# Kernel optimization log

Measured on AMD Instinct MI355X. Metric: run time of the kernel, lower is better.

Reference implementation:

```python
import jax, jax.numpy as jnp
import numpy as np

B, T, HIDDEN, CQ, CKV, NH, HD, RD = 4, 4096, 4096, 1536, 512, 32, 128, 64


def _rope(x):
    # x: (b, s, n, r); positions = arange(s) (decode step gets pos 0, matching
    # the module which passes no offset to RotaryPositionEmbedding)
    s, r = x.shape[1], x.shape[-1]
    inv_freq = 1.0 / (10000.0 ** (jnp.arange(0, r, 2, dtype=jnp.float32) / r))
    ang = jnp.arange(s, dtype=jnp.float32)[:, None] * inv_freq[None, :]  # (s, r/2)
    cos = jnp.cos(ang)[None, :, None, :].astype(x.dtype)
    sin = jnp.sin(ang)[None, :, None, :].astype(x.dtype)
    x1, x2 = x[..., ::2], x[..., 1::2]
    return jnp.stack([x1 * cos - x2 * sin, x1 * sin + x2 * cos], axis=-1).reshape(x.shape)


def setup_inputs() -> dict:
    key = jax.random.key(0)
    ks = jax.random.split(key, 12)
    wscale = jnp.float32(0.02)
    return {
        "hidden_states": jax.random.normal(ks[0], (B, 1, HIDDEN), jnp.float32),
        "mask": jnp.zeros((B, 1, NH, T + 1), jnp.float32),
        "cached_cKV": jax.random.normal(ks[1], (B, T, CKV), jnp.float32),
        "cached_kR": jax.random.normal(ks[2], (B, T, NH, RD), jnp.float32),
        "W_DQ": jax.random.normal(ks[3], (HIDDEN, CQ), jnp.float32) * wscale,
        "W_DKV": jax.random.normal(ks[4], (HIDDEN, CKV), jnp.float32) * wscale,
        "W_UQ_C": jax.random.normal(ks[5], (CQ, NH, HD), jnp.float32) * wscale,
        "W_UQ_R": jax.random.normal(ks[6], (CQ, NH, RD), jnp.float32) * wscale,
        "W_UK_C": jax.random.normal(ks[7], (CKV, NH, HD), jnp.float32) * wscale,
        "W_UV_C": jax.random.normal(ks[8], (CKV, NH, HD), jnp.float32) * wscale,
        "W_KR": jax.random.normal(ks[9], (HIDDEN, NH, RD), jnp.float32) * wscale,
        "W_O": jax.random.normal(ks[10], (NH, HD, HIDDEN), jnp.float32) * wscale,
    }


def reference(hidden_states, mask, cached_cKV, cached_kR,
              W_DQ, W_DKV, W_UQ_C, W_UQ_R, W_UK_C, W_UV_C, W_KR, W_O):
    Bc = hidden_states.shape[0]
    # query path
    cQ_t = jnp.einsum('bsh,hq->bsq', hidden_states, W_DQ)
    qC_t = jnp.einsum('bsq,qnd->bsnd', cQ_t, W_UQ_C)
    qR_t = jnp.einsum('bsq,qnr->bsnr', cQ_t, W_UQ_R)
    kR_t_raw = jnp.einsum('bsh,hnr->bsnr', hidden_states, W_KR)
    qR_t = _rope(qR_t)
    kR_t = _rope(kR_t_raw)
    # compressed KV for the new token
    cKV_t = jnp.einsum('bsh,hv->bsv', hidden_states, W_DKV)
    kC_t = jnp.einsum('bsv,vnd->bsnd', cKV_t, W_UK_C)
    vC_t = jnp.einsum('bsv,vnd->bsnd', cKV_t, W_UV_C)
    # decompress prefix cache and score
    prefix_len = cached_cKV.shape[1]
    kC_prefix = jnp.einsum('btv,vnd->btnd', cached_cKV, W_UK_C)   # (B,T,n,d)
    prefix_scores = (jnp.einsum('bsnd,btnd->bsnt', qC_t, kC_prefix)
                     + jnp.einsum('bsnr,btnr->bsnt', qR_t, cached_kR))
    new_score = (jnp.einsum('bsnd,bsnd->bsn', qC_t, kC_t)
                 + jnp.einsum('bsnr,bsnr->bsn', qR_t, kR_t))[..., None]
    attn_scores = jnp.concatenate([prefix_scores, new_score], axis=-1)
    scale = jnp.sqrt(jnp.float32(HD + RD)).astype(attn_scores.dtype)
    attn_scores = attn_scores / scale
    if mask is not None:
        attn_scores = attn_scores + mask * jnp.asarray(-1e9, attn_scores.dtype)
    attn_probs = jax.nn.softmax(attn_scores, axis=-1)
    # value aggregation
    vC_prefix = jnp.einsum('btv,vnd->btnd', cached_cKV, W_UV_C)
    prefix_agg = jnp.einsum('bsnt,btnd->bsnd', attn_probs[..., :prefix_len], vC_prefix)
    new_agg = attn_probs[..., -1:].reshape(Bc, 1, NH, 1) * vC_t
    attn_out = prefix_agg + new_agg
    output = jnp.einsum('bsnd,ndh->bsh', attn_out, W_O)
    new_cached_cKV = jnp.concatenate([cached_cKV, cKV_t], axis=1)
    new_cached_kR = jnp.concatenate([cached_kR, kR_t], axis=1)
    return (output, new_cached_cKV, new_cached_kR)
```

## Files before the change

### kernel.cpp

```cpp
#include <hip/hip_runtime.h>

#define TT 4096
#define T1 4097

using f32x4 = __attribute__((ext_vector_type(4))) float;

__device__ __forceinline__ void gemv_body(const float* __restrict__ X,
                                          const float* __restrict__ W,
                                          float* __restrict__ Y,
                                          int N, int K, int chunk, int ky) {
  const int tid = threadIdx.x;
  const int ct = tid & 7;
  const int kt = tid >> 3;
  const int col0 = blockIdx.x * 32 + ct * 4;
  const int k0 = ky * chunk;
  float acc[4][4];
#pragma unroll
  for (int c = 0; c < 4; ++c)
#pragma unroll
    for (int b = 0; b < 4; ++b) acc[c][b] = 0.f;
  const int iters = chunk >> 5;
  for (int i = 0; i < iters; ++i) {
    int k = k0 + kt + (i << 5);
    f32x4 w4 = *(const f32x4*)(W + (size_t)k * N + col0);
    float xb[4];
#pragma unroll
    for (int b = 0; b < 4; ++b) xb[b] = X[(size_t)b * K + k];
#pragma unroll
    for (int c = 0; c < 4; ++c)
#pragma unroll
      for (int b = 0; b < 4; ++b) acc[c][b] += w4[c] * xb[b];
  }
  __shared__ float red[256][16];
#pragma unroll
  for (int c = 0; c < 4; ++c)
#pragma unroll
    for (int b = 0; b < 4; ++b) red[tid][c * 4 + b] = acc[c][b];
  __syncthreads();
  for (int s = 16; s >= 1; s >>= 1) {
    if (kt < s) {
#pragma unroll
      for (int j = 0; j < 16; ++j) red[tid][j] += red[tid + 8 * s][j];
    }
    __syncthreads();
  }
  if (kt == 0) {
#pragma unroll
    for (int c = 0; c < 4; ++c)
#pragma unroll
      for (int b = 0; b < 4; ++b)
        atomicAdd(&Y[(size_t)b * N + col0 + c], red[ct][c * 4 + b]);
  }
}

__global__ __launch_bounds__(256) void gemv_hidden(const float* __restrict__ X,
                                                   const float* __restrict__ W0,
                                                   const float* __restrict__ W1,
                                                   const float* __restrict__ W2,
                                                   float* __restrict__ Ybase) {
  const int z = blockIdx.z;
  const float* W = (z == 0) ? W0 : (z == 1) ? W1 : W2;
  const int N = (z == 0) ? 1536 : (z == 1) ? 512 : 2048;
  const int nb = (z == 0) ? 48 : (z == 1) ? 16 : 64;
  const size_t yoff = (z == 0) ? 0 : (z == 1) ? 6144 : 8192;
  if ((int)blockIdx.x >= nb) return;
  gemv_body(X, W, Ybase + yoff, N, 4096, 512, blockIdx.y);
}

__global__ __launch_bounds__(256) void gemv_cq(const float* __restrict__ X,
                                               const float* __restrict__ W0,
                                               const float* __restrict__ W1,
                                               float* __restrict__ Y0,
                                               float* __restrict__ Y1) {
  const int z = blockIdx.z;
  const float* W = (z == 0) ? W0 : W1;
  float* Y = (z == 0) ? Y0 : Y1;
  const int N = (z == 0) ? 4096 : 2048;
  const int nb = (z == 0) ? 128 : 64;
  if ((int)blockIdx.x >= nb) return;
  gemv_body(X, W, Y, N, 1536, 384, blockIdx.y);
}

__global__ __launch_bounds__(256) void gemv_atomic(const float* __restrict__ X,
                                                   const float* __restrict__ W,
                                                   float* __restrict__ Y,
                                                   int N, int K, int chunk) {
  gemv_body(X, W, Y, N, K, chunk, blockIdx.y);
}

__global__ __launch_bounds__(128) void absorb_kernel(const float* __restrict__ qC,
                                                     const float* __restrict__ W_UK,
                                                     float* __restrict__ q_abs,
                                                     float* __restrict__ qT) {
  const int n = blockIdx.x, vt = blockIdx.y;
  __shared__ float qs[4][128];
  for (int i = threadIdx.x; i < 512; i += 128)
    qs[i >> 7][i & 127] = qC[(size_t)(i >> 7) * 4096 + n * 128 + (i & 127)];
  __syncthreads();
  const int v = vt * 128 + threadIdx.x;
  const float* wp = W_UK + (size_t)v * 4096 + n * 128;
  float acc[4] = {0.f, 0.f, 0.f, 0.f};
#pragma unroll 8
  for (int c = 0; c < 32; ++c) {
    f32x4 w4 = *(const f32x4*)(wp + c * 4);
#pragma unroll
    for (int j = 0; j < 4; ++j)
#pragma unroll
      for (int b = 0; b < 4; ++b) acc[b] += qs[b][c * 4 + j] * w4[j];
  }
#pragma unroll
  for (int b = 0; b < 4; ++b) {
    q_abs[((size_t)(b * 32) + n) * 512 + v] = acc[b];
    qT[((size_t)b * 512 + v) * 32 + n] = acc[b];
  }
}

__global__ __launch_bounds__(64) void newtok_kernel(const float* __restrict__ q_abs,
                                                    const float* __restrict__ cKV_t,
                                                    const float* __restrict__ qR,
                                                    const float* __restrict__ kR_t,
                                                    const float* __restrict__ mask,
                                                    float* __restrict__ valT) {
  const int row = blockIdx.x;
  const int b = row >> 5, n = row & 31;
  const int l = threadIdx.x;
  const float* qa = q_abs + (size_t)row * 512;
  const float* ck = cKV_t + b * 512;
  float p = 0.f;
#pragma unroll
  for (int j = 0; j < 8; ++j) p += qa[l + 64 * j] * ck[l + 64 * j];
  p += qR[(size_t)b * 2048 + n * 64 + l] * kR_t[(size_t)b * 2048 + n * 64 + l];
#pragma unroll
  for (int s = 1; s < 64; s <<= 1) p += __shfl_xor(p, s);
  if (l == 0)
    valT[row] = p * 0.0721687836487032f + mask[(size_t)row * T1 + TT] * (-1e9f);
}

__global__ __launch_bounds__(256, 4) void scores_split(const float* __restrict__ cKV,
                                                       const float* __restrict__ kR,
                                                       const float* __restrict__ qT,
                                                       const float* __restrict__ qR,
                                                       float* __restrict__ scores,
                                                       float* __restrict__ scoresR,
                                                       float* __restrict__ out_ckv,
                                                       float* __restrict__ out_kr) {
  const int bid = blockIdx.x;
  const int idx = bid >> 1;
  const int tid = threadIdx.x;
  const int b = idx >> 9;
  const int t0 = (idx & 511) * 8;
  __shared__ float ck[8][516];
  if (bid & 1) {
    for (int i = tid; i < 1024; i += 256) {
      int tl = i >> 7, vq = i & 127;
      f32x4 v = *(const f32x4*)(cKV + ((size_t)b * TT + t0 + tl) * 512 + vq * 4);
      *(f32x4*)&ck[tl][vq * 4] = v;
      __builtin_nontemporal_store(v, (f32x4*)(out_ckv + ((size_t)b * T1 + t0 + tl) * 512 + vq * 4));
    }
    __syncthreads();
    const int tl = tid >> 5, n = tid & 31;
    const float* qtb = qT + (size_t)b * 16384 + n;
    float a = 0.f;
#pragma unroll 8
    for (int v = 0; v < 512; ++v) a += qtb[(size_t)v * 32] * ck[tl][v];
    scores[((size_t)(b * 32) + n) * T1 + t0 + tl] = a;
  } else {
    const int w = tid >> 6, l = tid & 63;
    f32x4 q[8];
#pragma unroll
    for (int k = 0; k < 8; ++k)
      q[k] = *(const f32x4*)(qR + (size_t)b * 2048 + l * 4 + k * 256);
    const int nbase = l >> 4;
    const int wlead = ((l & 15) == 0);
#pragma unroll
    for (int r = 0; r < 2; ++r) {
      const int t = t0 + w * 2 + r;
      const float* src = kR + ((size_t)b * TT + t) * 2048 + l * 4;
      float* dst = out_kr + ((size_t)b * T1 + t) * 2048 + l * 4;
      f32x4 v[8];
#pragma unroll
      for (int k = 0; k < 8; ++k) v[k] = *(const f32x4*)(src + k * 256);
#pragma unroll
      for (int k = 0; k < 8; ++k)
        __builtin_nontemporal_store(v[k], (f32x4*)(dst + k * 256));
      float p[8];
#pragma unroll
      for (int k = 0; k < 8; ++k)
        p[k] = (q[k][0] * v[k][0] + q[k][1] * v[k][1]) +
               (q[k][2] * v[k][2] + q[k][3] * v[k][3]);
#pragma unroll
      for (int k = 0; k < 8; ++k) {
        p[k] += __shfl_xor(p[k], 1);
        p[k] += __shfl_xor(p[k], 2);
        p[k] += __shfl_xor(p[k], 4);
        p[k] += __shfl_xor(p[k], 8);
      }
      if (wlead) {
#pragma unroll
        for (int k = 0; k < 8; ++k)
          scoresR[((size_t)(b * 32) + k * 4 + nbase) * T1 + t] = p[k];
      }
    }
  }
}

__global__ __launch_bounds__(256) void agg_part(const float* __restrict__ cKV,
                                                const float* __restrict__ scores,
                                                const float* __restrict__ scoresR,
                                                const float* __restrict__ mask,
                                                float* __restrict__ aggP,
                                                float* __restrict__ statsC,
                                                int tlen, int NC) {
  const int chunk = blockIdx.x, b = blockIdx.y, vh = blockIdx.z;
  const int tid = threadIdx.x;
  const int vg = tid & 31, ng = tid >> 5;
  const float isc = 0.0721687836487032f;
  __shared__ float p_lds[32 * 129];
  __shared__ float gm[32], gs[32], scl[32];
  if (tid < 32) { gm[tid] = -1e30f; gs[tid] = 0.f; }
  float acc[4][4];
#pragma unroll
  for (int a = 0; a < 4; ++a)
#pragma unroll
    for (int j = 0; j < 4; ++j) acc[a][j] = 0.f;
  const int sub = (tlen < 128) ? tlen : 128;
  const int sshift = (sub == 64) ? 6 : 7;
  for (int tt = 0; tt < tlen; tt += sub) {
    const int t0 = chunk * tlen + tt;
    __syncthreads();
    for (int i = tid; i < (sub << 5); i += 256) {
      int nn = i >> sshift, tl = i & (sub - 1);
      size_t row = (size_t)(b * 32) + nn;
      size_t off = row * T1 + t0 + tl;
      p_lds[nn * 129 + tl] = (scores[off] + scoresR[off]) * isc + mask[off] * (-1e9f);
    }
    __syncthreads();
    {
      const int n8 = tid >> 3, lane = tid & 7;
      float mx = -1e30f;
      for (int t = lane; t < sub; t += 8) mx = fmaxf(mx, p_lds[n8 * 129 + t]);
      mx = fmaxf(mx, __shfl_xor(mx, 1));
      mx = fmaxf(mx, __shfl_xor(mx, 2));
      mx = fmaxf(mx, __shfl_xor(mx, 4));
      if (lane == 0) {
        float newM = fmaxf(gm[n8], mx);
        float sc = __expf(gm[n8] - newM);
        scl[n8] = sc;
        gm[n8] = newM;
        gs[n8] *= sc;
      }
    }
    __syncthreads();
#pragma unroll
    for (int a = 0; a < 4; ++a) {
      float sc = scl[ng * 4 + a];
#pragma unroll
      for (int j = 0; j < 4; ++j) acc[a][j] *= sc;
    }
    for (int i = tid; i < (sub << 5); i += 256) {
      int nn = i >> sshift, tl = i & (sub - 1);
      p_lds[nn * 129 + tl] = __expf(p_lds[nn * 129 + tl] - gm[nn]);
    }
    __syncthreads();
    {
      const int n8 = tid >> 3, lane = tid & 7;
      float se = 0.f;
      for (int t = lane; t < sub; t += 8) se += p_lds[n8 * 129 + t];
      se += __shfl_xor(se, 1);
      se += __shfl_xor(se, 2);
      se += __shfl_xor(se, 4);
      if (lane == 0) gs[n8] += se;
    }
    const float* cbase = cKV + ((size_t)b * TT + t0) * 512 + vh * 128 + vg * 4;
    for (int t = 0; t < sub; t += 2) {
      f32x4 c0 = *(const f32x4*)(cbase + (size_t)t * 512);
      f32x4 c1 = *(const f32x4*)(cbase + (size_t)(t + 1) * 512);
#pragma unroll
      for (int a = 0; a < 4; ++a) {
        float p0 = p_lds[(ng * 4 + a) * 129 + t];
        float p1 = p_lds[(ng * 4 + a) * 129 + t + 1];
#pragma unroll
        for (int j = 0; j < 4; ++j) acc[a][j] += p0 * c0[j] + p1 * c1[j];
      }
    }
  }
  __syncthreads();
#pragma unroll
  for (int a = 0; a < 4; ++a) {
    int n = ng * 4 + a;
    float* dst = aggP + (((size_t)b * NC + chunk) * 32 + n) * 512 + vh * 128 + vg * 4;
    f32x4 v;
#pragma unroll
    for (int j = 0; j < 4; ++j) v[j] = acc[a][j];
    *(f32x4*)dst = v;
  }
  if (vh == 0 && tid < 32) {
    size_t o = ((size_t)(b * 32) + tid) * NC + chunk;
    statsC[2 * o] = gm[tid];
    statsC[2 * o + 1] = gs[tid];
  }
}

__global__ __launch_bounds__(64) void stats_merge(const float* __restrict__ statsC,
                                                  const float* __restrict__ valT,
                                                  float* __restrict__ fact,
                                                  float* __restrict__ fT, int NC) {
  const int row = blockIdx.x;
  const int l = threadIdx.x;
  const float vt = valT[row];
  float mc = -1e30f, sc = 0.f;
  if (l < NC) {
    mc = statsC[2 * ((size_t)row * NC + l)];
    sc = statsC[2 * ((size_t)row * NC + l) + 1];
  }
  float m = fmaxf(mc, vt);
#pragma unroll
  for (int s = 1; s < 64; s <<= 1) m = fmaxf(m, __shfl_xor(m, s));
  float e = (l < NC) ? sc * __expf(mc - m) : 0.f;
  float S = e;
#pragma unroll
  for (int s = 1; s < 64; s <<= 1) S += __shfl_xor(S, s);
  S += __expf(vt - m);
  const float invS = 1.0f / S;
  if (l < NC) fact[(size_t)row * NC + l] = __expf(mc - m) * invS;
  if (l == 0) fT[row] = __expf(vt - m) * invS;
}

__global__ __launch_bounds__(256) void agg_reduce(const float* __restrict__ aggP,
                                                  const float* __restrict__ fact,
                                                  const float* __restrict__ fT,
                                                  const float* __restrict__ cKV_t,
                                                  float* __restrict__ agg, int NC) {
  const int idx = blockIdx.x * 256 + threadIdx.x;
  const int b = idx >> 14;
  const int n = (idx >> 9) & 31;
  const int v = idx & 511;
  const size_t row = (size_t)(b * 32) + n;
  float s = fT[row] * cKV_t[b * 512 + v];
  const float* pp = aggP + (((size_t)b * NC) * 32 + n) * 512 + v;
  const float* fc = fact + row * NC;
#pragma unroll 4
  for (int c = 0; c < NC; ++c) s += pp[(size_t)c * 32 * 512] * fc[c];
  agg[idx] = s;
}

__global__ __launch_bounds__(256) void out1_kernel(const float* __restrict__ agg,
                                                   const float* __restrict__ W_UV,
                                                   float* __restrict__ attn_out) {
  const int n = blockIdx.x, vc = blockIdx.y;
  const int tid = threadIdx.x;
  const int d = tid & 127, bh = tid >> 7;
  const float* a0 = agg + ((size_t)(bh * 32) + n) * 512;
  const float* a1 = agg + ((size_t)((bh + 2) * 32) + n) * 512;
  float acc0 = 0.f, acc1 = 0.f;
#pragma unroll 4
  for (int vv = 0; vv < 64; ++vv) {
    int v = vc * 64 + vv;
    float w = W_UV[(size_t)v * 4096 + n * 128 + d];
    acc0 += a0[v] * w;
    acc1 += a1[v] * w;
  }
  atomicAdd(&attn_out[(size_t)bh * 4096 + n * 128 + d], acc0);
  atomicAdd(&attn_out[(size_t)(bh + 2) * 4096 + n * 128 + d], acc1);
}

__global__ __launch_bounds__(256) void finalize_kernel(const float* __restrict__ outf,
                                                       const float* __restrict__ cKV_t,
                                                       const float* __restrict__ kR_t,
                                                       float* __restrict__ out) {
  int idx = blockIdx.x * 256 + threadIdx.x;
  if (idx < 16384) {
    out[idx] = outf[idx];
    return;
  }
  idx -= 16384;
  if (idx < 2048) {
    int b = idx >> 9, v = idx & 511;
    out[16384 + ((size_t)b * T1 + TT) * 512 + v] = cKV_t[idx];
    return;
  }
  idx -= 2048;
  if (idx < 8192) {
    int b = idx >> 11;
    int c = idx & 2047;
    out[16384 + (size_t)8390656 + ((size_t)b * T1 + TT) * 2048 + c] = kR_t[idx];
  }
}

extern "C" void kernel_launch(void* const* d_in, const int* in_sizes, int n_in,
                              void* d_out, int out_size, void* d_ws, size_t ws_size,
                              hipStream_t stream) {
  (void)in_sizes; (void)n_in; (void)out_size;
  const float* hidden = (const float*)d_in[0];
  const float* mask   = (const float*)d_in[1];
  const float* cKV    = (const float*)d_in[2];
  const float* kR     = (const float*)d_in[3];
  const float* W_DQ   = (const float*)d_in[4];
  const float* W_DKV  = (const float*)d_in[5];
  const float* W_UQ_C = (const float*)d_in[6];
  const float* W_UQ_R = (const float*)d_in[7];
  const float* W_UK_C = (const float*)d_in[8];
  const float* W_UV_C = (const float*)d_in[9];
  const float* W_KR   = (const float*)d_in[10];
  const float* W_O    = (const float*)d_in[11];

  float* ws = (float*)d_ws;
  const size_t WS_CQ = 0;
  const size_t WS_CKVT = 6144;
  const size_t WS_KRT = 8192;
  const size_t WS_QC = 16384;
  const size_t WS_QR = 32768;
  const size_t WS_OUTF = 40960;
  const size_t WS_ATTN = 57344;
  const size_t WS_VALT = 73728;
  const size_t WS_AGG = 74240;
  const size_t WS_QABS = 139776;
  const size_t WS_QT = 205312;
  const size_t WS_SCORES = 270848;
  const size_t WS_SCR = 795264;
  const size_t WS_STATSC = 1319680;
  const size_t WS_FACT = 1336064;
  const size_t WS_FT = 1344256;
  const size_t WS_AGGP = 1344512;

  int NC = 8;
  if (ws_size >= (WS_AGGP + (size_t)64 * 65536) * 4) NC = 64;
  else if (ws_size >= (WS_AGGP + (size_t)32 * 65536) * 4) NC = 32;
  else if (ws_size >= (WS_AGGP + (size_t)16 * 65536) * 4) NC = 16;
  const int tlen = 4096 / NC;

  float* out0 = (float*)d_out;
  float* out_ckv = out0 + 16384;
  float* out_kr = out_ckv + (size_t)8390656;

  hipMemsetAsync(d_ws, 0, 73728 * sizeof(float), stream);

  gemv_hidden<<<dim3(64, 8, 3), 256, 0, stream>>>(hidden, W_DQ, W_DKV, W_KR, ws);
  gemv_cq<<<dim3(128, 4, 2), 256, 0, stream>>>(ws + WS_CQ, W_UQ_C, W_UQ_R,
                                               ws + WS_QC, ws + WS_QR);
  absorb_kernel<<<dim3(32, 4), 128, 0, stream>>>(ws + WS_QC, W_UK_C, ws + WS_QABS, ws + WS_QT);
  newtok_kernel<<<128, 64, 0, stream>>>(ws + WS_QABS, ws + WS_CKVT, ws + WS_QR,
                                        ws + WS_KRT, mask, ws + WS_VALT);
  scores_split<<<4096, 256, 0, stream>>>(cKV, kR, ws + WS_QT, ws + WS_QR,
                                         ws + WS_SCORES, ws + WS_SCR, out_ckv, out_kr);
  agg_part<<<dim3(NC, 4, 4), 256, 0, stream>>>(cKV, ws + WS_SCORES, ws + WS_SCR, mask,
                                               ws + WS_AGGP, ws + WS_STATSC, tlen, NC);
  stats_merge<<<128, 64, 0, stream>>>(ws + WS_STATSC, ws + WS_VALT, ws + WS_FACT,
                                      ws + WS_FT, NC);
  agg_reduce<<<256, 256, 0, stream>>>(ws + WS_AGGP, ws + WS_FACT, ws + WS_FT,
                                      ws + WS_CKVT, ws + WS_AGG, NC);
  out1_kernel<<<dim3(32, 8), 256, 0, stream>>>(ws + WS_AGG, W_UV_C, ws + WS_ATTN);
  gemv_atomic<<<dim3(128, 8), 256, 0, stream>>>(ws + WS_ATTN, W_O, ws + WS_OUTF, 4096, 4096, 512);
  finalize_kernel<<<104, 256, 0, stream>>>(ws + WS_OUTF, ws + WS_CKVT, ws + WS_KRT, out0);
}
```

Measured before the change: 194.9 us.

## Fuse compressed-KV score computation into flash-style aggregation kernel

Moves the cKV·q_absorbed score computation out of the split scores kernel and into the aggregation kernel. Each block stages 16 cKV rows in shared memory, computes the scores there, and reuses the same tile for value aggregation. This removes the intermediate scores buffer write and re-read, and reads cKV once instead of twice. The tradeoff is that each of the 4 vh blocks recomputes the full score, so score FLOPs grow 4x. Occupancy may also drop because of the larger shared-memory footprint with small 16-token tiles.

```diff
diff --git a/kernel.cpp b/kernel.cpp
--- a/kernel.cpp
+++ b/kernel.cpp
@@ -136,86 +136,66 @@
     valT[row] = p * 0.0721687836487032f + mask[(size_t)row * T1 + TT] * (-1e9f);
 }
 
-__global__ __launch_bounds__(256, 4) void scores_split(const float* __restrict__ cKV,
-                                                       const float* __restrict__ kR,
-                                                       const float* __restrict__ qT,
-                                                       const float* __restrict__ qR,
-                                                       float* __restrict__ scores,
-                                                       float* __restrict__ scoresR,
-                                                       float* __restrict__ out_ckv,
-                                                       float* __restrict__ out_kr) {
-  const int bid = blockIdx.x;
-  const int idx = bid >> 1;
+__global__ __launch_bounds__(256, 4) void kr_scores(const float* __restrict__ kR,
+                                                    const float* __restrict__ qR,
+                                                    float* __restrict__ scoresR,
+                                                    float* __restrict__ out_kr) {
+  const int idx = blockIdx.x;
   const int tid = threadIdx.x;
   const int b = idx >> 9;
   const int t0 = (idx & 511) * 8;
-  __shared__ float ck[8][516];
-  if (bid & 1) {
-    for (int i = tid; i < 1024; i += 256) {
-      int tl = i >> 7, vq = i & 127;
-      f32x4 v = *(const f32x4*)(cKV + ((size_t)b * TT + t0 + tl) * 512 + vq * 4);
-      *(f32x4*)&ck[tl][vq * 4] = v;
-      __builtin_nontemporal_store(v, (f32x4*)(out_ckv + ((size_t)b * T1 + t0 + tl) * 512 + vq * 4));
-    }
-    __syncthreads();
-    const int tl = tid >> 5, n = tid & 31;
-    const float* qtb = qT + (size_t)b * 16384 + n;
-    float a = 0.f;
-#pragma unroll 8
-    for (int v = 0; v < 512; ++v) a += qtb[(size_t)v * 32] * ck[tl][v];
-    scores[((size_t)(b * 32) + n) * T1 + t0 + tl] = a;
-  } else {
-    const int w = tid >> 6, l = tid & 63;
-    f32x4 q[8];
+  const int w = tid >> 6, l = tid & 63;
+  f32x4 q[8];
+#pragma unroll
+  for (int k = 0; k < 8; ++k)
+    q[k] = *(const f32x4*)(qR + (size_t)b * 2048 + l * 4 + k * 256);
+  const int nbase = l >> 4;
+  const int wlead = ((l & 15) == 0);
+#pragma unroll
+  for (int r = 0; r < 2; ++r) {
+    const int t = t0 + w * 2 + r;
+    const float* src = kR + ((size_t)b * TT + t) * 2048 + l * 4;
+    float* dst = out_kr + ((size_t)b * T1 + t) * 2048 + l * 4;
+    f32x4 v[8];
+#pragma unroll
+    for (int k = 0; k < 8; ++k) v[k] = *(const f32x4*)(src + k * 256);
 #pragma unroll
     for (int k = 0; k < 8; ++k)
-      q[k] = *(const f32x4*)(qR + (size_t)b * 2048 + l * 4 + k * 256);
-    const int nbase = l >> 4;
-    const int wlead = ((l & 15) == 0);
-#pragma unroll
-    for (int r = 0; r < 2; ++r) {
-      const int t = t0 + w * 2 + r;
-      const float* src = kR + ((size_t)b * TT + t) * 2048 + l * 4;
-      float* dst = out_kr + ((size_t)b * T1 + t) * 2048 + l * 4;
-      f32x4 v[8];
-#pragma unroll
-      for (int k = 0; k < 8; ++k) v[k] = *(const f32x4*)(src + k * 256);
+      __builtin_nontemporal_store(v[k], (f32x4*)(dst + k * 256));
+    float p[8];
+#pragma unroll
+    for (int k = 0; k < 8; ++k)
+      p[k] = (q[k][0] * v[k][0] + q[k][1] * v[k][1]) +
+             (q[k][2] * v[k][2] + q[k][3] * v[k][3]);
+#pragma unroll
+    for (int k = 0; k < 8; ++k) {
+      p[k] += __shfl_xor(p[k], 1);
+      p[k] += __shfl_xor(p[k], 2);
+      p[k] += __shfl_xor(p[k], 4);
+      p[k] += __shfl_xor(p[k], 8);
+    }
+    if (wlead) {
 #pragma unroll
       for (int k = 0; k < 8; ++k)
-        __builtin_nontemporal_store(v[k], (f32x4*)(dst + k * 256));
-      float p[8];
-#pragma unroll
-      for (int k = 0; k < 8; ++k)
-        p[k] = (q[k][0] * v[k][0] + q[k][1] * v[k][1]) +
-               (q[k][2] * v[k][2] + q[k][3] * v[k][3]);
-#pragma unroll
-      for (int k = 0; k < 8; ++k) {
-        p[k] += __shfl_xor(p[k], 1);
-        p[k] += __shfl_xor(p[k], 2);
-        p[k] += __shfl_xor(p[k], 4);
-        p[k] += __shfl_xor(p[k], 8);
-      }
-      if (wlead) {
-#pragma unroll
-        for (int k = 0; k < 8; ++k)
-          scoresR[((size_t)(b * 32) + k * 4 + nbase) * T1 + t] = p[k];
-      }
-    }
-  }
-}
-
-__global__ __launch_bounds__(256) void agg_part(const float* __restrict__ cKV,
-                                                const float* __restrict__ scores,
-                                                const float* __restrict__ scoresR,
-                                                const float* __restrict__ mask,
-                                                float* __restrict__ aggP,
-                                                float* __restrict__ statsC,
-                                                int tlen, int NC) {
+        scoresR[((size_t)(b * 32) + k * 4 + nbase) * T1 + t] = p[k];
+    }
+  }
+}
+
+__global__ __launch_bounds__(256) void flash_agg(const float* __restrict__ cKV,
+                                                 const float* __restrict__ scoresR,
+                                                 const float* __restrict__ mask,
+                                                 const float* __restrict__ qT,
+                                                 float* __restrict__ out_ckv,
+                                                 float* __restrict__ aggP,
+                                                 float* __restrict__ statsC,
+                                                 int tlen, int NC) {
   const int chunk = blockIdx.x, b = blockIdx.y, vh = blockIdx.z;
   const int tid = threadIdx.x;
   const int vg = tid & 31, ng = tid >> 5;
   const float isc = 0.0721687836487032f;
-  __shared__ float p_lds[32 * 129];
+  __shared__ float ck[16 * 516];
+  __shared__ float p_lds[32 * 17];
   __shared__ float gm[32], gs[32], scl[32];
   if (tid < 32) { gm[tid] = -1e30f; gs[tid] = 0.f; }
   float acc[4][4];
@@ -223,22 +203,38 @@
   for (int a = 0; a < 4; ++a)
 #pragma unroll
     for (int j = 0; j < 4; ++j) acc[a][j] = 0.f;
-  const int sub = (tlen < 128) ? tlen : 128;
-  const int sshift = (sub == 64) ? 6 : 7;
-  for (int tt = 0; tt < tlen; tt += sub) {
+  for (int tt = 0; tt < tlen; tt += 16) {
     const int t0 = chunk * tlen + tt;
     __syncthreads();
-    for (int i = tid; i < (sub << 5); i += 256) {
-      int nn = i >> sshift, tl = i & (sub - 1);
-      size_t row = (size_t)(b * 32) + nn;
-      size_t off = row * T1 + t0 + tl;
-      p_lds[nn * 129 + tl] = (scores[off] + scoresR[off]) * isc + mask[off] * (-1e9f);
+    for (int i = tid; i < 2048; i += 256) {
+      int tl = i >> 7, vq = i & 127;
+      f32x4 v = *(const f32x4*)(cKV + ((size_t)b * TT + t0 + tl) * 512 + vq * 4);
+      *(f32x4*)&ck[tl * 516 + vq * 4] = v;
+      if (vh == 0)
+        __builtin_nontemporal_store(v, (f32x4*)(out_ckv + ((size_t)b * T1 + t0 + tl) * 512 + vq * 4));
+    }
+    __syncthreads();
+    {
+      const int t16 = tid >> 4, nn = tid & 15;
+      const float* qp = qT + (size_t)b * 16384 + nn * 2;
+      const float* cp = &ck[t16 * 516];
+      float s0 = 0.f, s1 = 0.f;
+#pragma unroll 8
+      for (int v = 0; v < 512; ++v) {
+        float cv = cp[v];
+        s0 += qp[(size_t)v * 32] * cv;
+        s1 += qp[(size_t)v * 32 + 1] * cv;
+      }
+      const int t = t0 + t16;
+      const size_t r0 = ((size_t)(b * 32) + nn * 2) * T1 + t;
+      const size_t r1 = r0 + T1;
+      p_lds[(nn * 2) * 17 + t16] = (s0 + scoresR[r0]) * isc + mask[r0] * (-1e9f);
+      p_lds[(nn * 2 + 1) * 17 + t16] = (s1 + scoresR[r1]) * isc + mask[r1] * (-1e9f);
     }
     __syncthreads();
     {
       const int n8 = tid >> 3, lane = tid & 7;
-      float mx = -1e30f;
-      for (int t = lane; t < sub; t += 8) mx = fmaxf(mx, p_lds[n8 * 129 + t]);
+      float mx = fmaxf(p_lds[n8 * 17 + lane], p_lds[n8 * 17 + lane + 8]);
       mx = fmaxf(mx, __shfl_xor(mx, 1));
       mx = fmaxf(mx, __shfl_xor(mx, 2));
       mx = fmaxf(mx, __shfl_xor(mx, 4));
@@ -257,30 +253,28 @@
 #pragma unroll
       for (int j = 0; j < 4; ++j) acc[a][j] *= sc;
     }
-    for (int i = tid; i < (sub << 5); i += 256) {
-      int nn = i >> sshift, tl = i & (sub - 1);
-      p_lds[nn * 129 + tl] = __expf(p_lds[nn * 129 + tl] - gm[nn]);
+    for (int i = tid; i < 512; i += 256) {
+      int nn = i >> 4, tl = i & 15;
+      p_lds[nn * 17 + tl] = __expf(p_lds[nn * 17 + tl] - gm[nn]);
     }
     __syncthreads();
     {
       const int n8 = tid >> 3, lane = tid & 7;
-      float se = 0.f;
-      for (int t = lane; t < sub; t += 8) se += p_lds[n8 * 129 + t];
+      float se = p_lds[n8 * 17 + lane] + p_lds[n8 * 17 + lane + 8];
       se += __shfl_xor(se, 1);
       se += __shfl_xor(se, 2);
       se += __shfl_xor(se, 4);
       if (lane == 0) gs[n8] += se;
     }
-    const float* cbase = cKV + ((size_t)b * TT + t0) * 512 + vh * 128 + vg * 4;
-    for (int t = 0; t < sub; t += 2) {
-      f32x4 c0 = *(const f32x4*)(cbase + (size_t)t * 512);
-      f32x4 c1 = *(const f32x4*)(cbase + (size_t)(t + 1) * 512);
+    const float* vb = &ck[vh * 128 + vg * 4];
+#pragma unroll 4
+    for (int t = 0; t < 16; ++t) {
+      f32x4 c0 = *(const f32x4*)(vb + t * 516);
 #pragma unroll
       for (int a = 0; a < 4; ++a) {
-        float p0 = p_lds[(ng * 4 + a) * 129 + t];
-        float p1 = p_lds[(ng * 4 + a) * 129 + t + 1];
-#pragma unroll
-        for (int j = 0; j < 4; ++j) acc[a][j] += p0 * c0[j] + p1 * c1[j];
+        float p = p_lds[(ng * 4 + a) * 17 + t];
+#pragma unroll
+        for (int j = 0; j < 4; ++j) acc[a][j] += p * c0[j];
       }
     }
   }
@@ -416,12 +410,11 @@
   const size_t WS_AGG = 74240;
   const size_t WS_QABS = 139776;
   const size_t WS_QT = 205312;
-  const size_t WS_SCORES = 270848;
-  const size_t WS_SCR = 795264;
-  const size_t WS_STATSC = 1319680;
-  const size_t WS_FACT = 1336064;
-  const size_t WS_FT = 1344256;
-  const size_t WS_AGGP = 1344512;
+  const size_t WS_SCR = 270848;
+  const size_t WS_STATSC = 795264;
+  const size_t WS_FACT = 811648;
+  const size_t WS_FT = 819840;
+  const size_t WS_AGGP = 820096;
 
   int NC = 8;
   if (ws_size >= (WS_AGGP + (size_t)64 * 65536) * 4) NC = 64;
@@ -441,10 +434,10 @@
   absorb_kernel<<<dim3(32, 4), 128, 0, stream>>>(ws + WS_QC, W_UK_C, ws + WS_QABS, ws + WS_QT);
   newtok_kernel<<<128, 64, 0, stream>>>(ws + WS_QABS, ws + WS_CKVT, ws + WS_QR,
                                         ws + WS_KRT, mask, ws + WS_VALT);
-  scores_split<<<4096, 256, 0, stream>>>(cKV, kR, ws + WS_QT, ws + WS_QR,
-                                         ws + WS_SCORES, ws + WS_SCR, out_ckv, out_kr);
-  agg_part<<<dim3(NC, 4, 4), 256, 0, stream>>>(cKV, ws + WS_SCORES, ws + WS_SCR, mask,
-                                               ws + WS_AGGP, ws + WS_STATSC, tlen, NC);
+  kr_scores<<<2048, 256, 0, stream>>>(kR, ws + WS_QR, ws + WS_SCR, out_kr);
+  flash_agg<<<dim3(NC, 4, 4), 256, 0, stream>>>(cKV, ws + WS_SCR, mask, ws + WS_QT,
+                                                out_ckv, ws + WS_AGGP, ws + WS_STATSC,
+                                                tlen, NC);
   stats_merge<<<128, 64, 0, stream>>>(ws + WS_STATSC, ws + WS_VALT, ws + WS_FACT,
                                       ws + WS_FT, NC);
   agg_reduce<<<256, 256, 0, stream>>>(ws + WS_AGGP, ws + WS_FACT, ws + WS_FT,
```

Result: slower. 395.1 us (+102.7%).
